# Kernel optimization log

Hardware: AMD Instinct MI355X
Metric: run time of the kernel (lower is better)

## Reference

```python
import jax, jax.numpy as jnp
import numpy as np
from jax import lax

SOS_TOKEN = 0
PAD_LEN = 30  # tokenizer.pad_len -> number of greedy decode steps


def _gru_cell(x, h, w_ih, w_hh, b_ih, b_hh):
    # PyTorch GRU cell math. x,h: [B,H]; w_*: [3H,H]; b_*: [3H]
    gi = x @ w_ih.T + b_ih
    gh = h @ w_hh.T + b_hh
    i_r, i_z, i_n = jnp.split(gi, 3, axis=-1)
    h_r, h_z, h_n = jnp.split(gh, 3, axis=-1)
    r = jax.nn.sigmoid(i_r + h_r)
    z = jax.nn.sigmoid(i_z + h_z)
    n = jnp.tanh(i_n + r * h_n)
    return (1.0 - z) * n + z * h


def _sm_encode(sm_hidden, conv_w, conv_b, enc_w, enc_b):
    # sm_hidden: [B, L, C] -> conv over time with C input channels
    x = jnp.transpose(sm_hidden, (0, 2, 1))  # [B, C, L]
    conv = lax.conv_general_dilated(
        x, conv_w, window_strides=(1,), padding='VALID',
        dimension_numbers=('NCH', 'OIH', 'NCH'))  # [B, O, L-k+1]
    conv = jax.nn.relu(conv + conv_b[None, :, None])
    pooled = jnp.max(conv, axis=-1)  # [B, O]
    return jax.nn.relu(pooled @ enc_w.T + enc_b)  # [B, H]


def reference(sm_hidden, embedding, w_ih, w_hh, b_ih, b_hh,
              w_out, b_out, conv_w, conv_b, enc_w, enc_b):
    B = sm_hidden.shape[0]
    h0 = _sm_encode(sm_hidden, conv_w, conv_b, enc_w, enc_b)  # [B, H]

    # The original re-runs the GRU over the whole (append-only) prefix each
    # iteration; since the GRU is deterministic this equals incremental
    # single-step updates, which we do here.
    def step(carry, _):
        h, tok = carry
        emb = embedding[tok]                      # [B, H]
        h_new = _gru_cell(emb, h, w_ih, w_hh, b_ih, b_hh)
        logits = h_new @ w_out.T + b_out          # [B, V]
        tok_new = jnp.argmax(logits, axis=-1)     # greedy topk(1)
        return (h_new, tok_new), (h_new, tok_new)

    tok0 = jnp.full((B,), SOS_TOKEN, dtype=jnp.int32)
    (h_last, _), (hiddens, toks) = lax.scan(step, (h0, tok0), None, length=PAD_LEN)

    decoder_output = jax.nn.log_softmax(h_last @ w_out.T + b_out, axis=1)  # [B, V]
    decoder_hidden = hiddens  # [PAD_LEN, B, H] == rnn_out of final _base_forward
    decoded_indices = jnp.concatenate([tok0[None, :], toks], axis=0)  # [PAD_LEN+1, B]
    return decoder_output, decoder_hidden, decoded_indices


def setup_inputs() -> dict:
    key = jax.random.key(0)
    ks = jax.random.split(key, 12)
    B, L, C = 512, 120, 128
    H, V, O, K = 1024, 512, 32, 10
    s = 1.0 / np.sqrt(H)
    return {
        'sm_hidden': jax.random.normal(ks[0], (B, L, C), jnp.float32),
        'embedding': jax.random.normal(ks[1], (V, H), jnp.float32),
        'w_ih': jax.random.uniform(ks[2], (3 * H, H), jnp.float32, -s, s),
        'w_hh': jax.random.uniform(ks[3], (3 * H, H), jnp.float32, -s, s),
        'b_ih': jax.random.uniform(ks[4], (3 * H,), jnp.float32, -s, s),
        'b_hh': jax.random.uniform(ks[5], (3 * H,), jnp.float32, -s, s),
        'w_out': jax.random.uniform(ks[6], (V, H), jnp.float32, -s, s),
        'b_out': jax.random.uniform(ks[7], (V,), jnp.float32, -s, s),
        'conv_w': jax.random.normal(ks[8], (O, C, K), jnp.float32) * 0.05,
        'conv_b': jax.random.normal(ks[9], (O,), jnp.float32) * 0.05,
        'enc_w': jax.random.uniform(ks[10], (H, O), jnp.float32, -s, s),
        'enc_b': jax.random.uniform(ks[11], (H,), jnp.float32, -s, s),
    }
```

## Files before the change

### kernel.cpp

```cpp
#include <hip/hip_runtime.h>
#include <hip/hip_bf16.h>
#include <math.h>

#define Bsz 512
#define Hd 1024
#define Vd 512
#define Cc 128
#define Ll 120
#define Kk 10
#define Oo 32
#define NSTEP 30

typedef __attribute__((ext_vector_type(8))) short bf16x8;
typedef __attribute__((ext_vector_type(4))) float f32x4;
typedef unsigned short ushort;

static __device__ __forceinline__ float sigm(float x) { return 1.f / (1.f + expf(-x)); }
static __device__ __forceinline__ ushort f2bf(float x) {
    __hip_bfloat16 h = __float2bfloat16(x);
    return *(ushort*)&h;
}
static __device__ __forceinline__ float bf2f(ushort u) {
    __hip_bfloat16 h; *(ushort*)&h = u;
    return __bfloat162float(h);
}

__global__ void k_split(const float* __restrict__ in, ushort* __restrict__ hi,
                        ushort* __restrict__ lo, int n) {
    int i = blockIdx.x * 256 + threadIdx.x;
    if (i < n) {
        float v = in[i];
        ushort h = f2bf(v);
        hi[i] = h;
        lo[i] = f2bf(v - bf2f(h));
    }
}

__global__ void k_pack(const float* __restrict__ W, ushort* __restrict__ hi,
                       ushort* __restrict__ lo, int total) {
    int idx = blockIdx.x * 256 + threadIdx.x;
    if (idx >= total) return;
    int jj = idx & 7, l = (idx >> 3) & 63, c = (idx >> 9) & 31, nf = idx >> 14;
    int n = nf * 16 + (l & 15);
    int k = c * 32 + ((l >> 4) << 3) + jj;
    float v = W[(size_t)n * 1024 + k];
    ushort h = f2bf(v);
    hi[idx] = h;
    lo[idx] = f2bf(v - bf2f(h));
}

__global__ void k_packconv(const float* __restrict__ cw, ushort* __restrict__ hi,
                           ushort* __restrict__ lo) {
    int idx = blockIdx.x * 256 + threadIdx.x;
    if (idx >= 2 * 40 * 64 * 8) return;
    int jj = idx & 7, l = (idx >> 3) & 63, ch = (idx >> 9) % 40, nf = idx / (40 * 512);
    int o = nf * 16 + (l & 15);
    int k = ch * 32 + ((l >> 4) << 3) + jj;
    int kc = k >> 7, c = k & 127;
    float v = cw[(o * Cc + c) * Kk + kc];
    ushort h = f2bf(v);
    hi[idx] = h;
    lo[idx] = f2bf(v - bf2f(h));
}

__global__ __launch_bounds__(256) void k_convmfma(const ushort* __restrict__ xH,
                                                  const ushort* __restrict__ xL,
                                                  const ushort* __restrict__ wH,
                                                  const ushort* __restrict__ wL,
                                                  const float* __restrict__ cb,
                                                  const float* __restrict__ ew,
                                                  const float* __restrict__ eb,
                                                  float* __restrict__ h0,
                                                  ushort* __restrict__ ApHi,
                                                  ushort* __restrict__ ApLo) {
    __shared__ float sred[4][2][16];
    __shared__ float ps[Oo];
    int b = blockIdx.x, tid = threadIdx.x, wid = tid >> 6, l = tid & 63;
    f32x4 acc[2][2];
#pragma unroll
    for (int i = 0; i < 2; ++i)
#pragma unroll
        for (int j = 0; j < 2; ++j) acc[i][j] = (f32x4)0.f;

    bf16x8 aH0[2], aL0[2], bH0[2], bL0[2];
    bf16x8 aH1[2], aL1[2], bH1[2], bL1[2];

#define CLD(AH, AL, BH, BL, ch)                                                        \
    {                                                                                  \
        _Pragma("unroll") for (int tf2 = 0; tf2 < 2; ++tf2) {                          \
            int aoff = ((b * 120 + (wid * 2 + tf2) * 16 + (l & 15) + ((ch) >> 2)) * 128 \
                        + ((ch) & 3) * 32 + ((l >> 4) << 3));                          \
            AH[tf2] = *(const bf16x8*)(xH + aoff);                                     \
            AL[tf2] = *(const bf16x8*)(xL + aoff);                                     \
        }                                                                              \
        _Pragma("unroll") for (int nf = 0; nf < 2; ++nf) {                             \
            int boff = ((nf * 40 + (ch)) * 64 + l) * 8;                                \
            BH[nf] = *(const bf16x8*)(wH + boff);                                      \
            BL[nf] = *(const bf16x8*)(wL + boff);                                      \
        }                                                                              \
    }
#define CST(AH, AL, BH, BL)                                                            \
    {                                                                                  \
        _Pragma("unroll") for (int tf2 = 0; tf2 < 2; ++tf2)                            \
            _Pragma("unroll") for (int nf = 0; nf < 2; ++nf) {                         \
                acc[tf2][nf] = __builtin_amdgcn_mfma_f32_16x16x32_bf16(                \
                    AH[tf2], BH[nf], acc[tf2][nf], 0, 0, 0);                           \
                acc[tf2][nf] = __builtin_amdgcn_mfma_f32_16x16x32_bf16(                \
                    AH[tf2], BL[nf], acc[tf2][nf], 0, 0, 0);                           \
                acc[tf2][nf] = __builtin_amdgcn_mfma_f32_16x16x32_bf16(                \
                    AL[tf2], BH[nf], acc[tf2][nf], 0, 0, 0);                           \
            }                                                                          \
    }

    CLD(aH0, aL0, bH0, bL0, 0)
#pragma unroll
    for (int ch = 0; ch < 40; ch += 2) {
        CLD(aH1, aL1, bH1, bL1, ch + 1)
        CST(aH0, aL0, bH0, bL0)
        if (ch + 2 < 40) CLD(aH0, aL0, bH0, bL0, ch + 2)
        CST(aH1, aL1, bH1, bL1)
    }
#undef CLD
#undef CST

    float mx[2] = {-1e38f, -1e38f};
#pragma unroll
    for (int tf2 = 0; tf2 < 2; ++tf2) {
        int tb = (wid * 2 + tf2) * 16 + ((l >> 4) << 2);
#pragma unroll
        for (int q = 0; q < 4; ++q) {
            if (tb + q <= 110) {
                mx[0] = fmaxf(mx[0], acc[tf2][0][q]);
                mx[1] = fmaxf(mx[1], acc[tf2][1][q]);
            }
        }
    }
#pragma unroll
    for (int s = 16; s < 64; s <<= 1) {
        mx[0] = fmaxf(mx[0], __shfl_xor(mx[0], s));
        mx[1] = fmaxf(mx[1], __shfl_xor(mx[1], s));
    }
    if (l < 16) {
        sred[wid][0][l] = mx[0];
        sred[wid][1][l] = mx[1];
    }
    __syncthreads();
    if (tid < Oo) {
        float m = sred[0][tid >> 4][tid & 15];
#pragma unroll
        for (int w = 1; w < 4; ++w) m = fmaxf(m, sred[w][tid >> 4][tid & 15]);
        ps[tid] = fmaxf(m + cb[tid], 0.f);
    }
    __syncthreads();
    for (int j = tid; j < Hd; j += 256) {
        float a = eb[j];
        const float4* e4 = (const float4*)(ew + (size_t)j * Oo);
#pragma unroll
        for (int c4 = 0; c4 < 8; ++c4) {
            float4 w = e4[c4];
            a += ps[c4 * 4 + 0] * w.x + ps[c4 * 4 + 1] * w.y +
                 ps[c4 * 4 + 2] * w.z + ps[c4 * 4 + 3] * w.w;
        }
        a = fmaxf(a, 0.f);
        h0[(size_t)b * Hd + j] = a;
        ushort hb = f2bf(a);
        ushort lb = f2bf(a - bf2f(hb));
        int c = j >> 5, sub = (j >> 3) & 3, jj = j & 7, mf = b >> 4;
        int lane_r = (b & 15) + (sub << 4);
        int flat = ((mf * 32 + c) * 64 + lane_r) * 8 + jj;
        ApHi[flat] = hb;
        ApLo[flat] = lb;
    }
}

template <int EPI>
__global__ __launch_bounds__(512, 2) void k_rnn(const ushort* __restrict__ Ah,
                                                const ushort* __restrict__ Al,
                                                const ushort* __restrict__ Bh,
                                                const ushort* __restrict__ Bl,
                                                const float* __restrict__ bias,
                                                float* __restrict__ outF,
                                                const float* __restrict__ gi_all,
                                                const int* __restrict__ tok,
                                                const float* __restrict__ hOld,
                                                ushort* __restrict__ ApHi,
                                                ushort* __restrict__ ApLo) {
    __shared__ ushort Bs[2][48][512];
    int id = blockIdx.x;
    int xcd = id & 7, r = id >> 3;
    int jt = xcd * 4 + (r & 3);
    int mt = r >> 2;
    int tid = threadIdx.x, wid = tid >> 6, l = tid & 63;
    int wm = wid >> 1, wj = wid & 1;
    int mf = mt * 4 + wm;
    int jf = jt * 2 + wj;
    int jcol = jf * 16 + (l & 15);

    float giR[4][3], hR[4];
    int bR[4];
    if constexpr (EPI == 1) {
#pragma unroll
        for (int q = 0; q < 4; ++q) {
            bR[q] = mf * 16 + ((l >> 4) << 2) + q;
            int tkq = tok[bR[q]];
            const float* gi = gi_all + (size_t)tkq * 3072;
            giR[q][0] = gi[jcol];
            giR[q][1] = gi[1024 + jcol];
            giR[q][2] = gi[2048 + jcol];
            hR[q] = hOld[(size_t)bR[q] * 1024 + jcol];
        }
    }

    f32x4 acc[3];
#pragma unroll
    for (int g = 0; g < 3; ++g) acc[g] = (f32x4)0.f;

    bf16x8 stg[6], aH0[4], aL0[4], aH1[4], aL1[4];

#define STG_LD(it)                                                                     \
    {                                                                                  \
        _Pragma("unroll") for (int k = 0; k < 6; ++k) {                                \
            int u = wid + 8 * k;                                                       \
            int hl = u & 1, wjb = (u >> 1) & 1, g = (u >> 2) % 3, cu = u / 12;         \
            const ushort* sp = hl ? Bl : Bh;                                           \
            stg[k] = *(const bf16x8*)(sp +                                             \
                (size_t)(((g * 64 + jt * 2 + wjb) * 32 + (it) * 4 + cu) * 64 + l) * 8);\
        }                                                                              \
    }
#define STG_WR(buf)                                                                    \
    {                                                                                  \
        _Pragma("unroll") for (int k = 0; k < 6; ++k)                                  \
            *(bf16x8*)&Bs[buf][wid + 8 * k][l * 8] = stg[k];                           \
    }
#define A_LD(DH, DL, it)                                                               \
    {                                                                                  \
        _Pragma("unroll") for (int cc = 0; cc < 4; ++cc) {                             \
            DH[cc] = *(const bf16x8*)(Ah + (size_t)((mf * 32 + (it) * 4 + cc) * 64 + l) * 8); \
            DL[cc] = *(const bf16x8*)(Al + (size_t)((mf * 32 + (it) * 4 + cc) * 64 + l) * 8); \
        }                                                                              \
    }
#define CMP(buf, AH, AL)                                                               \
    {                                                                                  \
        _Pragma("unroll") for (int cc = 0; cc < 4; ++cc)                               \
            _Pragma("unroll") for (int g = 0; g < 3; ++g) {                            \
                bf16x8 bhh = *(const bf16x8*)&Bs[buf][cc * 12 + g * 4 + wj * 2 + 0][l * 8]; \
                bf16x8 bll = *(const bf16x8*)&Bs[buf][cc * 12 + g * 4 + wj * 2 + 1][l * 8]; \
                acc[g] = __builtin_amdgcn_mfma_f32_16x16x32_bf16(AH[cc], bhh, acc[g], 0, 0, 0); \
                acc[g] = __builtin_amdgcn_mfma_f32_16x16x32_bf16(AH[cc], bll, acc[g], 0, 0, 0); \
                acc[g] = __builtin_amdgcn_mfma_f32_16x16x32_bf16(AL[cc], bhh, acc[g], 0, 0, 0); \
            }                                                                          \
    }

    STG_LD(0)
    STG_WR(0)
    STG_LD(1)
    A_LD(aH0, aL0, 0)
    __syncthreads();
#pragma unroll
    for (int it = 0; it < 8; ++it) {
        int buf = it & 1;
        if (it < 7) STG_WR(buf ^ 1)
        if (it < 6) STG_LD(it + 2)
        if (it & 1) {
            if (it < 7) A_LD(aH0, aL0, it + 1)
            CMP(buf, aH1, aL1)
        } else {
            if (it < 7) A_LD(aH1, aL1, it + 1)
            CMP(buf, aH0, aL0)
        }
        __syncthreads();
    }
#undef STG_LD
#undef STG_WR
#undef A_LD
#undef CMP

    if constexpr (EPI == 0) {
#pragma unroll
        for (int q = 0; q < 4; ++q) {
            int b = mf * 16 + ((l >> 4) << 2) + q;
#pragma unroll
            for (int g = 0; g < 3; ++g)
                outF[(size_t)b * 3072 + g * 1024 + jcol] =
                    acc[g][q] + bias[g * 1024 + jcol];
        }
    } else {
        float bj0 = bias[jcol], bj1 = bias[1024 + jcol], bj2 = bias[2048 + jcol];
        int c = jcol >> 5, sub = (jcol >> 3) & 3, jj = jcol & 7;
#pragma unroll
        for (int q = 0; q < 4; ++q) {
            int b = bR[q];
            float rr = sigm(giR[q][0] + acc[0][q] + bj0);
            float zz = sigm(giR[q][1] + acc[1][q] + bj1);
            float nn = tanhf(giR[q][2] + rr * (acc[2][q] + bj2));
            float hv = (1.f - zz) * nn + zz * hR[q];
            outF[(size_t)b * 1024 + jcol] = hv;
            ushort hb = f2bf(hv);
            ushort lb = f2bf(hv - bf2f(hb));
            int lane_r = (b & 15) + (sub << 4);
            int flat = ((mf * 32 + c) * 64 + lane_r) * 8 + jj;
            ApHi[flat] = hb;
            ApLo[flat] = lb;
        }
    }
}

__global__ __launch_bounds__(256) void k_lgt(const ushort* __restrict__ Ah,
                                             const ushort* __restrict__ Al,
                                             const ushort* __restrict__ Bh,
                                             const ushort* __restrict__ Bl,
                                             const float* __restrict__ bias,
                                             float* __restrict__ outF) {
    int p = blockIdx.x * 4 + (threadIdx.x >> 6);
    int l = threadIdx.x & 63;
    int mf = p >> 5, vf = p & 31;
    size_t ab = (size_t)(mf * 32) * 512 + l * 8;
    size_t bb = (size_t)(vf * 32) * 512 + l * 8;
    f32x4 acc = (f32x4)0.f;
    bf16x8 a0h, a0l, b0h, b0l, a1h, a1l, b1h, b1l;

#define LD1(AH, AL, BH, BL, c)                                                         \
    {                                                                                  \
        AH = *(const bf16x8*)(Ah + ab + (size_t)(c) * 512);                            \
        AL = *(const bf16x8*)(Al + ab + (size_t)(c) * 512);                            \
        BH = *(const bf16x8*)(Bh + bb + (size_t)(c) * 512);                            \
        BL = *(const bf16x8*)(Bl + bb + (size_t)(c) * 512);                            \
    }
#define ST1(AH, AL, BH, BL)                                                            \
    {                                                                                  \
        acc = __builtin_amdgcn_mfma_f32_16x16x32_bf16(AH, BH, acc, 0, 0, 0);           \
        acc = __builtin_amdgcn_mfma_f32_16x16x32_bf16(AH, BL, acc, 0, 0, 0);           \
        acc = __builtin_amdgcn_mfma_f32_16x16x32_bf16(AL, BH, acc, 0, 0, 0);           \
    }

    LD1(a0h, a0l, b0h, b0l, 0)
#pragma unroll
    for (int c = 0; c < 32; c += 2) {
        LD1(a1h, a1l, b1h, b1l, c + 1)
        ST1(a0h, a0l, b0h, b0l)
        if (c + 2 < 32) LD1(a0h, a0l, b0h, b0l, c + 2)
        ST1(a1h, a1l, b1h, b1l)
    }
#undef LD1
#undef ST1

    int v = vf * 16 + (l & 15);
    float bv = bias[v];
#pragma unroll
    for (int q = 0; q < 4; ++q) {
        int b = mf * 16 + ((l >> 4) << 2) + q;
        outF[(size_t)b * Vd + v] = acc[q] + bv;
    }
}

__global__ __launch_bounds__(64) void k_argmax(const float* __restrict__ logits,
                                               int* __restrict__ tok,
                                               float* __restrict__ out_idx,
                                               float* __restrict__ out_lsm,
                                               int do_lsm) {
    int b = blockIdx.x, l = threadIdx.x;
    const float* row = logits + (size_t)b * Vd;
    float bv = -3.4e38f;
    int bi = 0;
#pragma unroll
    for (int s = 0; s < 8; ++s) {
        int v = s * 64 + l;
        float x = row[v];
        if (x > bv) { bv = x; bi = v; }
    }
#pragma unroll
    for (int off = 1; off < 64; off <<= 1) {
        float ov = __shfl_xor(bv, off);
        int oi = __shfl_xor(bi, off);
        if (ov > bv || (ov == bv && oi < bi)) { bv = ov; bi = oi; }
    }
    if (l == 0) {
        tok[b] = bi;
        out_idx[b] = (float)bi;
    }
    if (do_lsm) {
        float sum = 0.f;
#pragma unroll
        for (int s = 0; s < 8; ++s) sum += expf(row[s * 64 + l] - bv);
#pragma unroll
        for (int off = 1; off < 64; off <<= 1) sum += __shfl_xor(sum, off);
        float lse = logf(sum) + bv;
#pragma unroll
        for (int s = 0; s < 8; ++s) {
            int v = s * 64 + l;
            out_lsm[(size_t)b * Vd + v] = row[v] - lse;
        }
    }
}

__global__ void k_init(int* __restrict__ tok, float* __restrict__ out_idx0) {
    int i = blockIdx.x * 64 + threadIdx.x;
    if (i < Bsz) {
        tok[i] = 0;
        out_idx0[i] = 0.f;
    }
}

extern "C" void kernel_launch(void* const* d_in, const int* in_sizes, int n_in,
                              void* d_out, int out_size, void* d_ws, size_t ws_size,
                              hipStream_t stream) {
    const float* sm    = (const float*)d_in[0];
    const float* emb   = (const float*)d_in[1];
    const float* w_ih  = (const float*)d_in[2];
    const float* w_hh  = (const float*)d_in[3];
    const float* b_ih  = (const float*)d_in[4];
    const float* b_hh  = (const float*)d_in[5];
    const float* w_out = (const float*)d_in[6];
    const float* b_out = (const float*)d_in[7];
    const float* cw    = (const float*)d_in[8];
    const float* cb    = (const float*)d_in[9];
    const float* ew    = (const float*)d_in[10];
    const float* eb    = (const float*)d_in[11];

    float* out0 = (float*)d_out;
    float* out1 = out0 + (size_t)Bsz * Vd;
    float* out2 = out1 + (size_t)NSTEP * Bsz * Hd;

    const int SMN = Bsz * Ll * Cc;
    char* wsp = (char*)d_ws;
    float*  f_gi  = (float*)wsp;  wsp += sizeof(float) * Bsz * 3072;
    float*  f_h0  = (float*)wsp;  wsp += sizeof(float) * Bsz * Hd;
    float*  f_log = (float*)wsp;  wsp += sizeof(float) * Bsz * Vd;
    ushort* ApHi0 = (ushort*)wsp; wsp += sizeof(ushort) * Bsz * Hd;
    ushort* ApLo0 = (ushort*)wsp; wsp += sizeof(ushort) * Bsz * Hd;
    ushort* ApHi1 = (ushort*)wsp; wsp += sizeof(ushort) * Bsz * Hd;
    ushort* ApLo1 = (ushort*)wsp; wsp += sizeof(ushort) * Bsz * Hd;
    ushort* embH  = (ushort*)wsp; wsp += sizeof(ushort) * Vd * Hd;
    ushort* embL  = (ushort*)wsp; wsp += sizeof(ushort) * Vd * Hd;
    ushort* wihH  = (ushort*)wsp; wsp += sizeof(ushort) * 3072 * Hd;
    ushort* wihL  = (ushort*)wsp; wsp += sizeof(ushort) * 3072 * Hd;
    ushort* whhH  = (ushort*)wsp; wsp += sizeof(ushort) * 3072 * Hd;
    ushort* whhL  = (ushort*)wsp; wsp += sizeof(ushort) * 3072 * Hd;
    ushort* woutH = (ushort*)wsp; wsp += sizeof(ushort) * Vd * Hd;
    ushort* woutL = (ushort*)wsp; wsp += sizeof(ushort) * Vd * Hd;
    ushort* smH   = (ushort*)wsp; wsp += sizeof(ushort) * (SMN + 32 * Cc);
    ushort* smL   = (ushort*)wsp; wsp += sizeof(ushort) * (SMN + 32 * Cc);
    ushort* cwBH  = (ushort*)wsp; wsp += sizeof(ushort) * 2 * 40 * 64 * 8;
    ushort* cwBL  = (ushort*)wsp; wsp += sizeof(ushort) * 2 * 40 * 64 * 8;
    int*    tok   = (int*)wsp;    wsp += sizeof(int) * Bsz;

    k_split<<<SMN / 256, 256, 0, stream>>>(sm, smH, smL, SMN);
    k_packconv<<<160, 256, 0, stream>>>(cw, cwBH, cwBL);
    k_pack<<<(3072 * 1024) / 256, 256, 0, stream>>>(w_ih, wihH, wihL, 3072 * 1024);
    k_pack<<<(3072 * 1024) / 256, 256, 0, stream>>>(w_hh, whhH, whhL, 3072 * 1024);
    k_pack<<<(512 * 1024) / 256, 256, 0, stream>>>(w_out, woutH, woutL, 512 * 1024);
    k_pack<<<(512 * 1024) / 256, 256, 0, stream>>>(emb, embH, embL, 512 * 1024);
    k_convmfma<<<Bsz, 256, 0, stream>>>(smH, smL, cwBH, cwBL, cb, ew, eb,
                                        f_h0, ApHi0, ApLo0);
    k_rnn<0><<<256, 512, 0, stream>>>(embH, embL, wihH, wihL, b_ih, f_gi,
                                      nullptr, nullptr, nullptr, nullptr, nullptr);
    k_init<<<8, 64, 0, stream>>>(tok, out2);

    ushort* aH[2] = {ApHi0, ApHi1};
    ushort* aL[2] = {ApLo0, ApLo1};
    for (int t = 0; t < NSTEP; ++t) {
        int cur = t & 1, nxt = cur ^ 1;
        const float* hOld = (t == 0) ? f_h0 : (out1 + (size_t)(t - 1) * Bsz * Hd);
        k_rnn<1><<<256, 512, 0, stream>>>(
            aH[cur], aL[cur], whhH, whhL, b_hh, out1 + (size_t)t * Bsz * Hd,
            f_gi, tok, hOld, aH[nxt], aL[nxt]);
        k_lgt<<<256, 256, 0, stream>>>(aH[nxt], aL[nxt], woutH, woutL, b_out, f_log);
        k_argmax<<<Bsz, 64, 0, stream>>>(f_log, tok, out2 + (size_t)(t + 1) * Bsz,
                                         out0, t == NSTEP - 1 ? 1 : 0);
    }
}
```

Measured before the change: 828.3 us.

## Fuse argmax into logits kernel via packed atomicMax and shrink RNN tiles

Removes the per-step argmax kernel by having the logits kernel reduce each 16-column tile and atomically max a packed (monotonic float, inverted index) 64-bit key per batch row. The next RNN step decodes the token from the packed key, resets the other buffer and writes the index output. A final kernel computes log-softmax once. Also halves the RNN LDS tile with more K iterations and raises the occupancy hint to 4 waves per SIMD, and makes the conv kernel process two batch rows per block. The changes trade one launch per step for global atomics and add register pressure risk under the tighter launch bounds.

```diff
diff --git a/kernel.cpp b/kernel.cpp
--- a/kernel.cpp
+++ b/kernel.cpp
@@ -14,6 +14,7 @@
 typedef __attribute__((ext_vector_type(8))) short bf16x8;
 typedef __attribute__((ext_vector_type(4))) float f32x4;
 typedef unsigned short ushort;
+typedef unsigned long long u64;
 
 static __device__ __forceinline__ float sigm(float x) { return 1.f / (1.f + expf(-x)); }
 static __device__ __forceinline__ ushort f2bf(float x) {
@@ -23,6 +24,10 @@
 static __device__ __forceinline__ float bf2f(ushort u) {
     __hip_bfloat16 h; *(ushort*)&h = u;
     return __bfloat162float(h);
+}
+static __device__ __forceinline__ unsigned monofy(float f) {
+    unsigned u = __float_as_uint(f);
+    return (u & 0x80000000u) ? ~u : (u | 0x80000000u);
 }
 
 __global__ void k_split(const float* __restrict__ in, ushort* __restrict__ hi,
@@ -75,15 +80,18 @@
                                                   ushort* __restrict__ ApLo) {
     __shared__ float sred[4][2][16];
     __shared__ float ps[Oo];
-    int b = blockIdx.x, tid = threadIdx.x, wid = tid >> 6, l = tid & 63;
-    f32x4 acc[2][2];
-#pragma unroll
-    for (int i = 0; i < 2; ++i)
-#pragma unroll
-        for (int j = 0; j < 2; ++j) acc[i][j] = (f32x4)0.f;
-
-    bf16x8 aH0[2], aL0[2], bH0[2], bL0[2];
-    bf16x8 aH1[2], aL1[2], bH1[2], bL1[2];
+    int tid = threadIdx.x, wid = tid >> 6, l = tid & 63;
+
+    for (int b2 = 0; b2 < 2; ++b2) {
+        int b = blockIdx.x * 2 + b2;
+        f32x4 acc[2][2];
+#pragma unroll
+        for (int i = 0; i < 2; ++i)
+#pragma unroll
+            for (int j = 0; j < 2; ++j) acc[i][j] = (f32x4)0.f;
+
+        bf16x8 aH0[2], aL0[2], bH0[2], bL0[2];
+        bf16x8 aH1[2], aL1[2], bH1[2], bL1[2];
 
 #define CLD(AH, AL, BH, BL, ch)                                                        \
     {                                                                                  \
@@ -112,80 +120,84 @@
             }                                                                          \
     }
 
-    CLD(aH0, aL0, bH0, bL0, 0)
-#pragma unroll
-    for (int ch = 0; ch < 40; ch += 2) {
-        CLD(aH1, aL1, bH1, bL1, ch + 1)
-        CST(aH0, aL0, bH0, bL0)
-        if (ch + 2 < 40) CLD(aH0, aL0, bH0, bL0, ch + 2)
-        CST(aH1, aL1, bH1, bL1)
-    }
+        CLD(aH0, aL0, bH0, bL0, 0)
+#pragma unroll
+        for (int ch = 0; ch < 40; ch += 2) {
+            CLD(aH1, aL1, bH1, bL1, ch + 1)
+            CST(aH0, aL0, bH0, bL0)
+            if (ch + 2 < 40) CLD(aH0, aL0, bH0, bL0, ch + 2)
+            CST(aH1, aL1, bH1, bL1)
+        }
 #undef CLD
 #undef CST
 
-    float mx[2] = {-1e38f, -1e38f};
-#pragma unroll
-    for (int tf2 = 0; tf2 < 2; ++tf2) {
-        int tb = (wid * 2 + tf2) * 16 + ((l >> 4) << 2);
-#pragma unroll
-        for (int q = 0; q < 4; ++q) {
-            if (tb + q <= 110) {
-                mx[0] = fmaxf(mx[0], acc[tf2][0][q]);
-                mx[1] = fmaxf(mx[1], acc[tf2][1][q]);
+        float mx[2] = {-1e38f, -1e38f};
+#pragma unroll
+        for (int tf2 = 0; tf2 < 2; ++tf2) {
+            int tb = (wid * 2 + tf2) * 16 + ((l >> 4) << 2);
+#pragma unroll
+            for (int q = 0; q < 4; ++q) {
+                if (tb + q <= 110) {
+                    mx[0] = fmaxf(mx[0], acc[tf2][0][q]);
+                    mx[1] = fmaxf(mx[1], acc[tf2][1][q]);
+                }
             }
         }
-    }
-#pragma unroll
-    for (int s = 16; s < 64; s <<= 1) {
-        mx[0] = fmaxf(mx[0], __shfl_xor(mx[0], s));
-        mx[1] = fmaxf(mx[1], __shfl_xor(mx[1], s));
-    }
-    if (l < 16) {
-        sred[wid][0][l] = mx[0];
-        sred[wid][1][l] = mx[1];
-    }
-    __syncthreads();
-    if (tid < Oo) {
-        float m = sred[0][tid >> 4][tid & 15];
-#pragma unroll
-        for (int w = 1; w < 4; ++w) m = fmaxf(m, sred[w][tid >> 4][tid & 15]);
-        ps[tid] = fmaxf(m + cb[tid], 0.f);
-    }
-    __syncthreads();
-    for (int j = tid; j < Hd; j += 256) {
-        float a = eb[j];
-        const float4* e4 = (const float4*)(ew + (size_t)j * Oo);
-#pragma unroll
-        for (int c4 = 0; c4 < 8; ++c4) {
-            float4 w = e4[c4];
-            a += ps[c4 * 4 + 0] * w.x + ps[c4 * 4 + 1] * w.y +
-                 ps[c4 * 4 + 2] * w.z + ps[c4 * 4 + 3] * w.w;
-        }
-        a = fmaxf(a, 0.f);
-        h0[(size_t)b * Hd + j] = a;
-        ushort hb = f2bf(a);
-        ushort lb = f2bf(a - bf2f(hb));
-        int c = j >> 5, sub = (j >> 3) & 3, jj = j & 7, mf = b >> 4;
-        int lane_r = (b & 15) + (sub << 4);
-        int flat = ((mf * 32 + c) * 64 + lane_r) * 8 + jj;
-        ApHi[flat] = hb;
-        ApLo[flat] = lb;
+#pragma unroll
+        for (int s = 16; s < 64; s <<= 1) {
+            mx[0] = fmaxf(mx[0], __shfl_xor(mx[0], s));
+            mx[1] = fmaxf(mx[1], __shfl_xor(mx[1], s));
+        }
+        if (l < 16) {
+            sred[wid][0][l] = mx[0];
+            sred[wid][1][l] = mx[1];
+        }
+        __syncthreads();
+        if (tid < Oo) {
+            float m = sred[0][tid >> 4][tid & 15];
+#pragma unroll
+            for (int w = 1; w < 4; ++w) m = fmaxf(m, sred[w][tid >> 4][tid & 15]);
+            ps[tid] = fmaxf(m + cb[tid], 0.f);
+        }
+        __syncthreads();
+        for (int j = tid; j < Hd; j += 256) {
+            float a = eb[j];
+            const float4* e4 = (const float4*)(ew + (size_t)j * Oo);
+#pragma unroll
+            for (int c4 = 0; c4 < 8; ++c4) {
+                float4 w = e4[c4];
+                a += ps[c4 * 4 + 0] * w.x + ps[c4 * 4 + 1] * w.y +
+                     ps[c4 * 4 + 2] * w.z + ps[c4 * 4 + 3] * w.w;
+            }
+            a = fmaxf(a, 0.f);
+            h0[(size_t)b * Hd + j] = a;
+            ushort hb = f2bf(a);
+            ushort lb = f2bf(a - bf2f(hb));
+            int c = j >> 5, sub = (j >> 3) & 3, jj = j & 7, mf = b >> 4;
+            int lane_r = (b & 15) + (sub << 4);
+            int flat = ((mf * 32 + c) * 64 + lane_r) * 8 + jj;
+            ApHi[flat] = hb;
+            ApLo[flat] = lb;
+        }
+        __syncthreads();
     }
 }
 
 template <int EPI>
-__global__ __launch_bounds__(512, 2) void k_rnn(const ushort* __restrict__ Ah,
+__global__ __launch_bounds__(512, 4) void k_rnn(const ushort* __restrict__ Ah,
                                                 const ushort* __restrict__ Al,
                                                 const ushort* __restrict__ Bh,
                                                 const ushort* __restrict__ Bl,
                                                 const float* __restrict__ bias,
                                                 float* __restrict__ outF,
                                                 const float* __restrict__ gi_all,
-                                                const int* __restrict__ tok,
+                                                const u64* __restrict__ pkRd,
+                                                u64* __restrict__ pkWr,
+                                                float* __restrict__ outIdxRow,
                                                 const float* __restrict__ hOld,
                                                 ushort* __restrict__ ApHi,
                                                 ushort* __restrict__ ApLo) {
-    __shared__ ushort Bs[2][48][512];
+    __shared__ ushort Bs[2][24][512];
     int id = blockIdx.x;
     int xcd = id & 7, r = id >> 3;
     int jt = xcd * 4 + (r & 3);
@@ -197,51 +209,59 @@
     int jcol = jf * 16 + (l & 15);
 
     float giR[4][3], hR[4];
-    int bR[4];
+    int bR[4], tkR[4];
     if constexpr (EPI == 1) {
 #pragma unroll
         for (int q = 0; q < 4; ++q) {
             bR[q] = mf * 16 + ((l >> 4) << 2) + q;
-            int tkq = tok[bR[q]];
-            const float* gi = gi_all + (size_t)tkq * 3072;
+            u64 pk = pkRd[bR[q]];
+            tkR[q] = 511 - (int)(unsigned)(pk & 0xFFFFFFFFu);
+            const float* gi = gi_all + (size_t)tkR[q] * 3072;
             giR[q][0] = gi[jcol];
             giR[q][1] = gi[1024 + jcol];
             giR[q][2] = gi[2048 + jcol];
             hR[q] = hOld[(size_t)bR[q] * 1024 + jcol];
         }
+        if (jt == 0 && wj == 0 && (l & 15) == 0) {
+#pragma unroll
+            for (int q = 0; q < 4; ++q) {
+                pkWr[bR[q]] = 0ULL;
+                if (outIdxRow) outIdxRow[bR[q]] = (float)tkR[q];
+            }
+        }
     }
 
     f32x4 acc[3];
 #pragma unroll
     for (int g = 0; g < 3; ++g) acc[g] = (f32x4)0.f;
 
-    bf16x8 stg[6], aH0[4], aL0[4], aH1[4], aL1[4];
+    bf16x8 stg[3], aH0[2], aL0[2], aH1[2], aL1[2];
 
 #define STG_LD(it)                                                                     \
     {                                                                                  \
-        _Pragma("unroll") for (int k = 0; k < 6; ++k) {                                \
+        _Pragma("unroll") for (int k = 0; k < 3; ++k) {                                \
             int u = wid + 8 * k;                                                       \
             int hl = u & 1, wjb = (u >> 1) & 1, g = (u >> 2) % 3, cu = u / 12;         \
             const ushort* sp = hl ? Bl : Bh;                                           \
             stg[k] = *(const bf16x8*)(sp +                                             \
-                (size_t)(((g * 64 + jt * 2 + wjb) * 32 + (it) * 4 + cu) * 64 + l) * 8);\
+                (size_t)(((g * 64 + jt * 2 + wjb) * 32 + (it) * 2 + cu) * 64 + l) * 8);\
         }                                                                              \
     }
 #define STG_WR(buf)                                                                    \
     {                                                                                  \
-        _Pragma("unroll") for (int k = 0; k < 6; ++k)                                  \
+        _Pragma("unroll") for (int k = 0; k < 3; ++k)                                  \
             *(bf16x8*)&Bs[buf][wid + 8 * k][l * 8] = stg[k];                           \
     }
 #define A_LD(DH, DL, it)                                                               \
     {                                                                                  \
-        _Pragma("unroll") for (int cc = 0; cc < 4; ++cc) {                             \
-            DH[cc] = *(const bf16x8*)(Ah + (size_t)((mf * 32 + (it) * 4 + cc) * 64 + l) * 8); \
-            DL[cc] = *(const bf16x8*)(Al + (size_t)((mf * 32 + (it) * 4 + cc) * 64 + l) * 8); \
+        _Pragma("unroll") for (int cc = 0; cc < 2; ++cc) {                             \
+            DH[cc] = *(const bf16x8*)(Ah + (size_t)((mf * 32 + (it) * 2 + cc) * 64 + l) * 8); \
+            DL[cc] = *(const bf16x8*)(Al + (size_t)((mf * 32 + (it) * 2 + cc) * 64 + l) * 8); \
         }                                                                              \
     }
 #define CMP(buf, AH, AL)                                                               \
     {                                                                                  \
-        _Pragma("unroll") for (int cc = 0; cc < 4; ++cc)                               \
+        _Pragma("unroll") for (int cc = 0; cc < 2; ++cc)                               \
             _Pragma("unroll") for (int g = 0; g < 3; ++g) {                            \
                 bf16x8 bhh = *(const bf16x8*)&Bs[buf][cc * 12 + g * 4 + wj * 2 + 0][l * 8]; \
                 bf16x8 bll = *(const bf16x8*)&Bs[buf][cc * 12 + g * 4 + wj * 2 + 1][l * 8]; \
@@ -257,15 +277,15 @@
     A_LD(aH0, aL0, 0)
     __syncthreads();
 #pragma unroll
-    for (int it = 0; it < 8; ++it) {
+    for (int it = 0; it < 16; ++it) {
         int buf = it & 1;
-        if (it < 7) STG_WR(buf ^ 1)
-        if (it < 6) STG_LD(it + 2)
+        if (it < 15) STG_WR(buf ^ 1)
+        if (it < 14) STG_LD(it + 2)
         if (it & 1) {
-            if (it < 7) A_LD(aH0, aL0, it + 1)
+            if (it < 15) A_LD(aH0, aL0, it + 1)
             CMP(buf, aH1, aL1)
         } else {
-            if (it < 7) A_LD(aH1, aL1, it + 1)
+            if (it < 15) A_LD(aH1, aL1, it + 1)
             CMP(buf, aH0, aL0)
         }
         __syncthreads();
@@ -310,7 +330,8 @@
                                              const ushort* __restrict__ Bh,
                                              const ushort* __restrict__ Bl,
                                              const float* __restrict__ bias,
-                                             float* __restrict__ outF) {
+                                             float* __restrict__ outF,
+                                             u64* __restrict__ pkOut) {
     int p = blockIdx.x * 4 + (threadIdx.x >> 6);
     int l = threadIdx.x & 63;
     int mf = p >> 5, vf = p & 31;
@@ -346,57 +367,64 @@
 
     int v = vf * 16 + (l & 15);
     float bv = bias[v];
+    float lg[4];
+    unsigned vmq[4];
 #pragma unroll
     for (int q = 0; q < 4; ++q) {
         int b = mf * 16 + ((l >> 4) << 2) + q;
-        outF[(size_t)b * Vd + v] = acc[q] + bv;
-    }
-}
-
-__global__ __launch_bounds__(64) void k_argmax(const float* __restrict__ logits,
-                                               int* __restrict__ tok,
-                                               float* __restrict__ out_idx,
-                                               float* __restrict__ out_lsm,
-                                               int do_lsm) {
+        lg[q] = acc[q] + bv;
+        outF[(size_t)b * Vd + v] = lg[q];
+        vmq[q] = 511u - (unsigned)v;
+    }
+#pragma unroll
+    for (int off = 1; off < 16; off <<= 1) {
+#pragma unroll
+        for (int q = 0; q < 4; ++q) {
+            float og = __shfl_xor(lg[q], off);
+            unsigned ov = __shfl_xor(vmq[q], off);
+            if (og > lg[q] || (og == lg[q] && ov > vmq[q])) { lg[q] = og; vmq[q] = ov; }
+        }
+    }
+    if ((l & 15) == 0) {
+#pragma unroll
+        for (int q = 0; q < 4; ++q) {
+            int b = mf * 16 + ((l >> 4) << 2) + q;
+            u64 pk = ((u64)monofy(lg[q]) << 32) | (u64)vmq[q];
+            atomicMax(&pkOut[b], pk);
+        }
+    }
+}
+
+__global__ __launch_bounds__(64) void k_fin(const float* __restrict__ logits,
+                                            const u64* __restrict__ pk,
+                                            float* __restrict__ out_lsm,
+                                            float* __restrict__ outIdxRow) {
     int b = blockIdx.x, l = threadIdx.x;
     const float* row = logits + (size_t)b * Vd;
     float bv = -3.4e38f;
-    int bi = 0;
+#pragma unroll
+    for (int s = 0; s < 8; ++s) bv = fmaxf(bv, row[s * 64 + l]);
+#pragma unroll
+    for (int off = 1; off < 64; off <<= 1) bv = fmaxf(bv, __shfl_xor(bv, off));
+    float sum = 0.f;
+#pragma unroll
+    for (int s = 0; s < 8; ++s) sum += expf(row[s * 64 + l] - bv);
+#pragma unroll
+    for (int off = 1; off < 64; off <<= 1) sum += __shfl_xor(sum, off);
+    float lse = logf(sum) + bv;
 #pragma unroll
     for (int s = 0; s < 8; ++s) {
         int v = s * 64 + l;
-        float x = row[v];
-        if (x > bv) { bv = x; bi = v; }
-    }
-#pragma unroll
-    for (int off = 1; off < 64; off <<= 1) {
-        float ov = __shfl_xor(bv, off);
-        int oi = __shfl_xor(bi, off);
-        if (ov > bv || (ov == bv && oi < bi)) { bv = ov; bi = oi; }
-    }
-    if (l == 0) {
-        tok[b] = bi;
-        out_idx[b] = (float)bi;
-    }
-    if (do_lsm) {
-        float sum = 0.f;
-#pragma unroll
-        for (int s = 0; s < 8; ++s) sum += expf(row[s * 64 + l] - bv);
-#pragma unroll
-        for (int off = 1; off < 64; off <<= 1) sum += __shfl_xor(sum, off);
-        float lse = logf(sum) + bv;
-#pragma unroll
-        for (int s = 0; s < 8; ++s) {
-            int v = s * 64 + l;
-            out_lsm[(size_t)b * Vd + v] = row[v] - lse;
-        }
-    }
-}
-
-__global__ void k_init(int* __restrict__ tok, float* __restrict__ out_idx0) {
+        out_lsm[(size_t)b * Vd + v] = row[v] - lse;
+    }
+    if (l == 0)
+        outIdxRow[b] = (float)(511 - (int)(unsigned)(pk[b] & 0xFFFFFFFFu));
+}
+
+__global__ void k_init(u64* __restrict__ P0, float* __restrict__ out_idx0) {
     int i = blockIdx.x * 64 + threadIdx.x;
     if (i < Bsz) {
-        tok[i] = 0;
+        P0[i] = (1ULL << 32) | 511ULL;
         out_idx0[i] = 0.f;
     }
 }
@@ -426,6 +454,8 @@
     float*  f_gi  = (float*)wsp;  wsp += sizeof(float) * Bsz * 3072;
     float*  f_h0  = (float*)wsp;  wsp += sizeof(float) * Bsz * Hd;
     float*  f_log = (float*)wsp;  wsp += sizeof(float) * Bsz * Vd;
+    u64*    Ppk0  = (u64*)wsp;    wsp += sizeof(u64) * Bsz;
+    u64*    Ppk1  = (u64*)wsp;    wsp += sizeof(u64) * Bsz;
     ushort* ApHi0 = (ushort*)wsp; wsp += sizeof(ushort) * Bsz * Hd;
     ushort* ApLo0 = (ushort*)wsp; wsp += sizeof(ushort) * Bsz * Hd;
     ushort* ApHi1 = (ushort*)wsp; wsp += sizeof(ushort) * Bsz * Hd;
@@ -442,7 +472,6 @@
     ushort* smL   = (ushort*)wsp; wsp += sizeof(ushort) * (SMN + 32 * Cc);
     ushort* cwBH  = (ushort*)wsp; wsp += sizeof(ushort) * 2 * 40 * 64 * 8;
     ushort* cwBL  = (ushort*)wsp; wsp += sizeof(ushort) * 2 * 40 * 64 * 8;
-    int*    tok   = (int*)wsp;    wsp += sizeof(int) * Bsz;
 
     k_split<<<SMN / 256, 256, 0, stream>>>(sm, smH, smL, SMN);
     k_packconv<<<160, 256, 0, stream>>>(cw, cwBH, cwBL);
@@ -450,22 +479,27 @@
     k_pack<<<(3072 * 1024) / 256, 256, 0, stream>>>(w_hh, whhH, whhL, 3072 * 1024);
     k_pack<<<(512 * 1024) / 256, 256, 0, stream>>>(w_out, woutH, woutL, 512 * 1024);
     k_pack<<<(512 * 1024) / 256, 256, 0, stream>>>(emb, embH, embL, 512 * 1024);
-    k_convmfma<<<Bsz, 256, 0, stream>>>(smH, smL, cwBH, cwBL, cb, ew, eb,
+    k_convmfma<<<256, 256, 0, stream>>>(smH, smL, cwBH, cwBL, cb, ew, eb,
                                         f_h0, ApHi0, ApLo0);
     k_rnn<0><<<256, 512, 0, stream>>>(embH, embL, wihH, wihL, b_ih, f_gi,
-                                      nullptr, nullptr, nullptr, nullptr, nullptr);
-    k_init<<<8, 64, 0, stream>>>(tok, out2);
+                                      nullptr, nullptr, nullptr, nullptr, nullptr,
+                                      nullptr, nullptr);
+    k_init<<<8, 64, 0, stream>>>(Ppk0, out2);
 
     ushort* aH[2] = {ApHi0, ApHi1};
     ushort* aL[2] = {ApLo0, ApLo1};
+    u64* P[2] = {Ppk0, Ppk1};
     for (int t = 0; t < NSTEP; ++t) {
         int cur = t & 1, nxt = cur ^ 1;
         const float* hOld = (t == 0) ? f_h0 : (out1 + (size_t)(t - 1) * Bsz * Hd);
         k_rnn<1><<<256, 512, 0, stream>>>(
             aH[cur], aL[cur], whhH, whhL, b_hh, out1 + (size_t)t * Bsz * Hd,
-            f_gi, tok, hOld, aH[nxt], aL[nxt]);
-        k_lgt<<<256, 256, 0, stream>>>(aH[nxt], aL[nxt], woutH, woutL, b_out, f_log);
-        k_argmax<<<Bsz, 64, 0, stream>>>(f_log, tok, out2 + (size_t)(t + 1) * Bsz,
-                                         out0, t == NSTEP - 1 ? 1 : 0);
-    }
-}
+            f_gi, P[t & 1], P[(t + 1) & 1],
+            (t >= 1) ? (out2 + (size_t)t * Bsz) : nullptr,
+            hOld, aH[nxt], aL[nxt]);
+        k_lgt<<<256, 256, 0, stream>>>(aH[nxt], aL[nxt], woutH, woutL, b_out,
+                                       f_log, P[(t + 1) & 1]);
+    }
+    k_fin<<<Bsz, 64, 0, stream>>>(f_log, P[NSTEP & 1], out0,
+                                  out2 + (size_t)NSTEP * Bsz);
+}
```

Measured after the change: 926.6 us. 1.12x slower.
